# Optimization experiments

Measured on AMD Instinct MI355X. Metric: run time of the kernel, lower is better.

The kernel has to match this reference:

```python
import jax, jax.numpy as jnp
import numpy as np

D_MODEL = 768; D_STATE = 64; D_CONV = 7; EXPAND = 2; HEADDIM = 64; NGROUPS = 1; CHUNK = 256
D_INNER = EXPAND * D_MODEL                                      # 1536
NHEADS = D_INNER // HEADDIM                                     # 24
D_IN_PROJ = 2 * D_INNER + 2 * NGROUPS * D_STATE + 2 * NHEADS    # 3248
CONV_DIM = D_INNER + 2 * NGROUPS * D_STATE                      # 1664
BATCH, SEQLEN = 2, 4096
EPS = 1e-5


def setup_inputs() -> dict:
    key = jax.random.key(0)
    ks = jax.random.split(key, 8)
    w = lambda k, shape, s=0.02: jax.random.normal(k, shape, jnp.float32) * s
    # dt in [1e-3, 1e-1], dt_bias = softplus^{-1}(dt)
    dt0 = jnp.exp(jax.random.uniform(ks[3], (NHEADS,)) * (np.log(0.1) - np.log(0.001)) + np.log(0.001))
    return {
        "x": jax.random.normal(ks[0], (BATCH, SEQLEN, D_MODEL), jnp.float32),
        "ln_w": jnp.ones((D_MODEL,), jnp.float32),
        "ln_b": jnp.zeros((D_MODEL,), jnp.float32),
        "in_proj_w": w(ks[1], (D_IN_PROJ, D_MODEL)),
        "conv_w": w(ks[2], (CONV_DIM, D_CONV), 0.2),
        "conv_b": jnp.zeros((CONV_DIM,), jnp.float32),
        "dt_bias": dt0 + jnp.log(-jnp.expm1(-dt0)),
        "A_log": jnp.log(jax.random.uniform(ks[4], (NHEADS,), minval=1.0, maxval=16.0)),
        "D": jnp.ones((NHEADS,), jnp.float32),
        "fc_D_w": w(ks[5], (NHEADS, D_INNER)),
        "rms_w": jnp.ones((D_INNER,), jnp.float32),
        "out_proj_w": w(ks[6], (D_MODEL, D_INNER)),
    }


def _segsum(a):
    # a: (..., T) -> (..., T, T) lower-triangular segment sums, -inf above diagonal
    T = a.shape[-1]
    cs = jnp.cumsum(a, -1)
    ss = cs[..., :, None] - cs[..., None, :]
    return jnp.where(jnp.tril(jnp.ones((T, T), bool)), ss, -jnp.inf)


def _ssd(X, A, Bm, Cm):
    # Chunked SSD scan (mamba_chunk_scan_combined, D=None, z=None, ngroups=1).
    # X: (b,l,h,p) already scaled by dt; A: (b,l,h) = dt*A_head; Bm,Cm: (b,l,n)
    b, l, h, p = X.shape
    c = l // CHUNK
    X = X.reshape(b, c, CHUNK, h, p)
    A = A.reshape(b, c, CHUNK, h).transpose(0, 3, 1, 2)  # (b,h,c,l)
    Bm = Bm.reshape(b, c, CHUNK, D_STATE)
    Cm = Cm.reshape(b, c, CHUNK, D_STATE)
    A_cum = jnp.cumsum(A, -1)
    Lmat = jnp.exp(_segsum(A))                                      # (b,h,c,l,s)
    Y_diag = jnp.einsum("bcln,bcsn,bhcls,bcshp->bclhp", Cm, Bm, Lmat, X)
    decay_states = jnp.exp(A_cum[..., -1:] - A_cum)                 # (b,h,c,l)
    states = jnp.einsum("bcln,bhcl,bclhp->bchpn", Bm, decay_states, X)
    A_chunk = jnp.pad(A_cum[..., -1], ((0, 0), (0, 0), (1, 0)))     # (b,h,c+1)
    decay_chunk = jnp.exp(_segsum(A_chunk))                         # (b,h,c+1,c+1)
    all_states = jnp.concatenate([jnp.zeros_like(states[:, :1]), states], 1)
    prev = jnp.einsum("bhzc,bchpn->bzhpn", decay_chunk, all_states)[:, :-1]
    Y_off = jnp.einsum("bcln,bchpn,bhcl->bclhp", Cm, prev, jnp.exp(A_cum))
    return (Y_diag + Y_off).reshape(b, l, h, p)


def _dwconv_causal(x, w, b):
    # x: (B,L,C), w: (C,K); torch Conv1d(padding=K-1) then [:, :L] == causal conv
    xp = jnp.pad(x, ((0, 0), (D_CONV - 1, 0), (0, 0))).transpose(0, 2, 1)
    y = jax.lax.conv_general_dilated(xp, w[:, None, :], (1,), "VALID",
                                     feature_group_count=CONV_DIM,
                                     dimension_numbers=("NCH", "OIH", "NCH"))
    return y.transpose(0, 2, 1) + b


def _forward(x, ln_w, ln_b, in_proj_w, conv_w, conv_b, dt_bias, A_log, D, fc_D_w, rms_w, out_proj_w):
    B, L, _ = x.shape
    # pre-LayerNorm
    mu = jnp.mean(x, -1, keepdims=True)
    var = jnp.mean((x - mu) ** 2, -1, keepdims=True)
    u = (x - mu) * jax.lax.rsqrt(var + EPS) * ln_w + ln_b
    # input projection -> z | xBC | dt_fw,dt_bw
    zxbcdt = u @ in_proj_w.T
    z = zxbcdt[..., :D_INNER]
    xBC = zxbcdt[..., D_INNER:D_INNER + CONV_DIM]
    dt2 = zxbcdt[..., -2 * NHEADS:]
    dt = jnp.concatenate([dt2[..., :NHEADS], jnp.flip(dt2[..., NHEADS:], 1)], 0)  # (2B,L,H)
    dt = jax.nn.softplus(dt + dt_bias)
    A = -jnp.exp(A_log)
    # causal depthwise conv + SiLU
    xBC = jax.nn.silu(_dwconv_causal(xBC, conv_w, conv_b))
    xs = xBC[..., :D_INNER]
    Bm = xBC[..., D_INNER:D_INNER + D_STATE]
    Cm = xBC[..., D_INNER + D_STATE:]
    x_og = xs
    cat2 = lambda t: jnp.concatenate([t, jnp.flip(t, 1)], 0)  # fwd + reversed copy
    X = cat2(xs).reshape(2 * B, L, NHEADS, HEADDIM) * dt[..., None]
    y = _ssd(X, dt * A, cat2(Bm), cat2(Cm)).reshape(2 * B, L, D_INNER)
    # quasiseparable combine: shift each direction by one, zero the boundary
    y = jnp.roll(y, 1, axis=1).at[:, 0, :].set(0.0)
    y = y[:B] + jnp.flip(y[B:], 1)
    # data-dependent diagonal term
    Dterm = x_og @ fc_D_w.T + D                                 # (B,L,H)
    y = y + x_og * jnp.repeat(Dterm, HEADDIM, axis=-1)
    # gated RMSNorm
    y = y * jax.nn.silu(z)
    y = y * jax.lax.rsqrt(jnp.mean(y * y, -1, keepdims=True) + EPS) * rms_w
    # out projection + residual (dropout=0 -> identity)
    return y @ out_proj_w.T + x


def reference(x, ln_w, ln_b, in_proj_w, conv_w, conv_b, dt_bias, A_log, D, fc_D_w, rms_w, out_proj_w):
    return _forward(x, ln_w, ln_b, in_proj_w, conv_w, conv_b, dt_bias, A_log, D, fc_D_w, rms_w, out_proj_w)
```

## Files before the change

kernel.cpp:

```cpp
#include <hip/hip_runtime.h>
#include <hip/hip_bf16.h>
#include <cstdint>
#include <cstddef>

typedef __hip_bfloat16 bf16;
typedef __attribute__((ext_vector_type(8))) short short8;
typedef __attribute__((ext_vector_type(4))) float f32x4;

#define B_   2
#define L_   4096
#define DM_  768
#define DI_  1536
#define NH_  24
#define HD_  64
#define DS_  64
#define CH_  256
#define NC_  16
#define CD_  1664
#define DIP_ 3248
#define NPAD_ 3328
#define EPS_ 1e-5f

#define ROWS_ (B_*L_)
#define BB4_  (2*B_)

#define LDT  72

__device__ __forceinline__ float b2f(bf16 v) { return __bfloat162float(v); }
__device__ __forceinline__ bf16  f2b(float v) { return __float2bfloat16(v); }
__device__ __forceinline__ float sb2f(short s) {
    bf16 t; __builtin_memcpy(&t, &s, 2); return __bfloat162float(t);
}
__device__ __forceinline__ short f2s(float v) {
    bf16 t = __float2bfloat16(v); short s; __builtin_memcpy(&s, &t, 2); return s;
}
__device__ __forceinline__ void gl_lds16(const void* g, void* l) {
    __builtin_amdgcn_global_load_lds((const __attribute__((address_space(1))) unsigned int*)g,
                                     (__attribute__((address_space(3))) unsigned int*)l,
                                     16, 0, 0);
}

__global__ __launch_bounds__(256) void cast_f2b(const float* __restrict__ s,
                                                bf16* __restrict__ d, int n) {
    int i = (blockIdx.x * 256 + threadIdx.x) * 4;
    if (i + 3 < n) {
        float4 v = *(const float4*)(s + i);
        d[i]   = f2b(v.x); d[i+1] = f2b(v.y);
        d[i+2] = f2b(v.z); d[i+3] = f2b(v.w);
    } else {
        for (int k = i; k < n; k++) d[k] = f2b(s[k]);
    }
}

__global__ __launch_bounds__(256) void cast_pad_inproj(const float* __restrict__ s,
                                                       bf16* __restrict__ d) {
    int i = (blockIdx.x * 256 + threadIdx.x) * 4;
    const int nsrc = DIP_ * DM_;
    const int ntot = NPAD_ * DM_;
    if (i >= ntot) return;
    if (i + 3 < nsrc) {
        float4 v = *(const float4*)(s + i);
        d[i]   = f2b(v.x); d[i+1] = f2b(v.y);
        d[i+2] = f2b(v.z); d[i+3] = f2b(v.w);
    } else {
        for (int k = i; k < i + 4 && k < ntot; k++)
            d[k] = (k < nsrc) ? f2b(s[k]) : f2b(0.f);
    }
}

__global__ __launch_bounds__(256) void ln_kernel(const float* __restrict__ x,
                                                 const float* __restrict__ w,
                                                 const float* __restrict__ bb,
                                                 bf16* __restrict__ u) {
    int row = blockIdx.x, tid = threadIdx.x;
    const float* xr = x + (size_t)row * DM_;
    float v0 = xr[tid], v1 = xr[tid + 256], v2 = xr[tid + 512];
    float s = v0 + v1 + v2;
    float q = v0*v0 + v1*v1 + v2*v2;
    for (int off = 32; off > 0; off >>= 1) {
        s += __shfl_down(s, off);
        q += __shfl_down(q, off);
    }
    __shared__ float rs[4], rq[4];
    __shared__ float mean_s, rstd_s;
    int lane = tid & 63, wid = tid >> 6;
    if (!lane) { rs[wid] = s; rq[wid] = q; }
    __syncthreads();
    if (!tid) {
        float S = rs[0]+rs[1]+rs[2]+rs[3];
        float Q = rq[0]+rq[1]+rq[2]+rq[3];
        float mu = S / (float)DM_;
        float var = Q / (float)DM_ - mu*mu;
        mean_s = mu; rstd_s = rsqrtf(var + EPS_);
    }
    __syncthreads();
    float mu = mean_s, rstd = rstd_s;
    bf16* ur = u + (size_t)row * DM_;
    ur[tid]       = f2b((v0 - mu) * rstd * w[tid]       + bb[tid]);
    ur[tid + 256] = f2b((v1 - mu) * rstd * w[tid + 256] + bb[tid + 256]);
    ur[tid + 512] = f2b((v2 - mu) * rstd * w[tid + 512] + bb[tid + 512]);
}

__global__ __launch_bounds__(256) void gemm_gl_inproj(const bf16* __restrict__ A,
                                                      const bf16* __restrict__ W,
                                                      bf16* __restrict__ zbuf,
                                                      bf16* __restrict__ xbc,
                                                      float* __restrict__ dtr) {
    __shared__ short As[128 * 32];
    __shared__ short Ws[128 * 32];
    int tid = threadIdx.x;
    int wave = tid >> 6, lane = tid & 63;
    int wm = (wave >> 1) * 64, wn = (wave & 1) * 64;
    int bm = blockIdx.y * 128, bn = blockIdx.x * 128;
    int fr = lane & 15, g = lane >> 4;
    const int K = DM_;
    int srow = lane >> 2;
    int scol = ((lane & 3) ^ ((lane >> 3) & 3)) * 8;
    int rsl = (g ^ ((fr >> 1) & 3)) * 8;
    const short* Ag = (const short*)A;
    const short* Wg = (const short*)W;
    f32x4 acc[4][4] = {};
    for (int k0 = 0; k0 < K; k0 += 32) {
        __syncthreads();
        #pragma unroll
        for (int q = 0; q < 2; q++) {
            gl_lds16(Ag + (size_t)(bm + q*64 + wave*16 + srow) * K + k0 + scol,
                     &As[(q*64 + wave*16) * 32]);
            gl_lds16(Wg + (size_t)(bn + q*64 + wave*16 + srow) * K + k0 + scol,
                     &Ws[(q*64 + wave*16) * 32]);
        }
        __syncthreads();
        short8 af[4], wf[4];
        #pragma unroll
        for (int i = 0; i < 4; i++)
            af[i] = *(const short8*)&As[(wm + i*16 + fr)*32 + rsl];
        #pragma unroll
        for (int j = 0; j < 4; j++)
            wf[j] = *(const short8*)&Ws[(wn + j*16 + fr)*32 + rsl];
        #pragma unroll
        for (int i = 0; i < 4; i++)
            #pragma unroll
            for (int j = 0; j < 4; j++)
                acc[i][j] = __builtin_amdgcn_mfma_f32_16x16x32_bf16(af[i], wf[j], acc[i][j], 0, 0, 0);
    }
    int rg = (lane >> 4) * 4;
    #pragma unroll
    for (int i = 0; i < 4; i++) {
        int mrow = bm + wm + i*16 + rg;
        #pragma unroll
        for (int j = 0; j < 4; j++) {
            int ncol = bn + wn + j*16 + fr;
            #pragma unroll
            for (int r = 0; r < 4; r++) {
                float v = acc[i][j][r];
                int m = mrow + r;
                if (ncol < DI_)            zbuf[(size_t)m * DI_ + ncol] = f2b(v);
                else if (ncol < DI_ + CD_) xbc[(size_t)m * CD_ + (ncol - DI_)] = f2b(v);
                else if (ncol < DIP_)      dtr[(size_t)m * 48 + (ncol - DI_ - CD_)] = v;
            }
        }
    }
}

__global__ __launch_bounds__(256) void gemm_gl_out(const bf16* __restrict__ A,
                                                   const bf16* __restrict__ W,
                                                   const float* __restrict__ resid,
                                                   float* __restrict__ C) {
    __shared__ short As[128 * 32];
    __shared__ short Ws[128 * 32];
    int tid = threadIdx.x;
    int wave = tid >> 6, lane = tid & 63;
    int wm = (wave >> 1) * 64, wn = (wave & 1) * 64;
    int bm = blockIdx.y * 128, bn = blockIdx.x * 128;
    int fr = lane & 15, g = lane >> 4;
    const int K = DI_;
    int srow = lane >> 2;
    int scol = ((lane & 3) ^ ((lane >> 3) & 3)) * 8;
    int rsl = (g ^ ((fr >> 1) & 3)) * 8;
    const short* Ag = (const short*)A;
    const short* Wg = (const short*)W;
    f32x4 acc[4][4] = {};
    for (int k0 = 0; k0 < K; k0 += 32) {
        __syncthreads();
        #pragma unroll
        for (int q = 0; q < 2; q++) {
            gl_lds16(Ag + (size_t)(bm + q*64 + wave*16 + srow) * K + k0 + scol,
                     &As[(q*64 + wave*16) * 32]);
            gl_lds16(Wg + (size_t)(bn + q*64 + wave*16 + srow) * K + k0 + scol,
                     &Ws[(q*64 + wave*16) * 32]);
        }
        __syncthreads();
        short8 af[4], wf[4];
        #pragma unroll
        for (int i = 0; i < 4; i++)
            af[i] = *(const short8*)&As[(wm + i*16 + fr)*32 + rsl];
        #pragma unroll
        for (int j = 0; j < 4; j++)
            wf[j] = *(const short8*)&Ws[(wn + j*16 + fr)*32 + rsl];
        #pragma unroll
        for (int i = 0; i < 4; i++)
            #pragma unroll
            for (int j = 0; j < 4; j++)
                acc[i][j] = __builtin_amdgcn_mfma_f32_16x16x32_bf16(af[i], wf[j], acc[i][j], 0, 0, 0);
    }
    int rg = (lane >> 4) * 4;
    #pragma unroll
    for (int i = 0; i < 4; i++) {
        int mrow = bm + wm + i*16 + rg;
        #pragma unroll
        for (int j = 0; j < 4; j++) {
            int ncol = bn + wn + j*16 + fr;
            #pragma unroll
            for (int r = 0; r < 4; r++) {
                int m = mrow + r;
                C[(size_t)m * DM_ + ncol] = acc[i][j][r] + resid[(size_t)m * DM_ + ncol];
            }
        }
    }
}

__global__ __launch_bounds__(256) void conv_kernel(const bf16* __restrict__ xbc,
                                                   const float* __restrict__ cw,
                                                   const float* __restrict__ cb,
                                                   bf16* __restrict__ out) {
    int g = blockIdx.x * 256 + threadIdx.x;
    int cg = g % 208;
    int tq = g / 208;
    int b = tq >> 10;
    int t0 = (tq & 1023) * 4;
    int c8 = cg * 8;
    const short* src = (const short*)xbc + (size_t)(b * L_) * CD_ + c8;

    float w[7][8], acc[4][8];
    #pragma unroll
    for (int k = 0; k < 8; k++) {
        #pragma unroll
        for (int j = 0; j < 7; j++) w[j][k] = cw[(c8 + k) * 7 + j];
        float bias = cb[c8 + k];
        #pragma unroll
        for (int q = 0; q < 4; q++) acc[q][k] = bias;
    }
    #pragma unroll
    for (int m = 0; m < 10; m++) {
        int tt = t0 - 6 + m;
        float row[8];
        if (tt >= 0) {
            short8 v = *(const short8*)(src + (size_t)tt * CD_);
            #pragma unroll
            for (int k = 0; k < 8; k++) row[k] = sb2f(v[k]);
        } else {
            #pragma unroll
            for (int k = 0; k < 8; k++) row[k] = 0.f;
        }
        #pragma unroll
        for (int q = 0; q < 4; q++) {
            int j = m - q;
            if (j >= 0 && j < 7) {
                #pragma unroll
                for (int k = 0; k < 8; k++) acc[q][k] += row[k] * w[j][k];
            }
        }
    }
    #pragma unroll
    for (int q = 0; q < 4; q++) {
        short8 o;
        #pragma unroll
        for (int k = 0; k < 8; k++) {
            float a = acc[q][k];
            a = a / (1.f + __expf(-a));
            o[k] = f2s(a);
        }
        *(short8*)((short*)out + (size_t)(b * L_ + t0 + q) * CD_ + c8) = o;
    }
}

__global__ __launch_bounds__(256) void dt_kernel(const float* __restrict__ dtr,
                                                 const float* __restrict__ dt_bias,
                                                 float* __restrict__ dt4) {
    int idx = blockIdx.x * 256 + threadIdx.x;
    if (idx >= BB4_ * L_ * NH_) return;
    int h = idx % NH_;
    int t = (idx / NH_) % L_;
    int bbx = idx / (NH_ * L_);
    int bp = bbx & 1;
    float raw;
    if (bbx < 2) raw = dtr[((size_t)(bp * L_ + t)) * 48 + h];
    else         raw = dtr[((size_t)(bp * L_ + (L_ - 1 - t))) * 48 + NH_ + h];
    float v = raw + dt_bias[h];
    float dt = (v > 20.f) ? v : log1pf(__expf(v));
    dt4[idx] = dt;
}

__global__ __launch_bounds__(256) void scan_kernel(const float* __restrict__ dt4,
                                                   const float* __restrict__ A_log,
                                                   float* __restrict__ Acum) {
    int bid = blockIdx.x;
    int c  = bid % NC_;
    int h  = (bid / NC_) % NH_;
    int bbx = bid / (NC_ * NH_);
    int l = threadIdx.x;
    float Ah = -__expf(A_log[h]);
    float val = dt4[((size_t)(bbx * L_) + c * CH_ + l) * NH_ + h] * Ah;
    __shared__ float sc[256];
    sc[l] = val; __syncthreads();
    for (int off = 1; off < 256; off <<= 1) {
        float t = (l >= off) ? sc[l - off] : 0.f;
        __syncthreads();
        sc[l] += t;
        __syncthreads();
    }
    Acum[(size_t)bid * CH_ + l] = sc[l];
}

__global__ __launch_bounds__(256) void xt_kernel(const bf16* __restrict__ conv,
                                                 const float* __restrict__ dt4,
                                                 bf16* __restrict__ XT,
                                                 bf16* __restrict__ BT) {
    int bid = blockIdx.x;
    int hh = bid % 25;
    int c  = (bid / 25) % NC_;
    int bbx = bid / (25 * NC_);
    int bp = bbx & 1;
    bool flip = bbx >= 2;
    bool isB = (hh == NH_);
    int coff = isB ? DI_ : hh * HD_;
    int tid = threadIdx.x;
    __shared__ short tile[64][72];
    short* dstb = (short*)(isB ? BT : XT);
    size_t rowbase = isB ? (size_t)(bbx * 64) : (size_t)((bbx * NH_ + hh) * 64);
    for (int lt = 0; lt < 4; lt++) {
        __syncthreads();
        #pragma unroll
        for (int it = 0; it < 2; it++) {
            int li = tid + it * 256;
            int r = li >> 3, seg = (li & 7) * 8;
            int t = c * CH_ + lt * 64 + r;
            int tt = flip ? (L_ - 1 - t) : t;
            short8 v = *(const short8*)((const short*)conv + (size_t)(bp * L_ + tt) * CD_ + coff + seg);
            if (!isB) {
                float dtv = dt4[((size_t)(bbx * L_) + t) * NH_ + hh];
                #pragma unroll
                for (int k = 0; k < 8; k++) v[k] = f2s(sb2f(v[k]) * dtv);
            }
            *(short8*)&tile[r][seg] = v;
        }
        __syncthreads();
        #pragma unroll
        for (int it = 0; it < 2; it++) {
            int li = tid + it * 256;
            int p = li >> 3, seg = (li & 7) * 8;
            short8 o;
            #pragma unroll
            for (int k = 0; k < 8; k++) o[k] = tile[seg + k][p];
            *(short8*)(dstb + (rowbase + p) * L_ + c * CH_ + lt * 64 + seg) = o;
        }
    }
}

__global__ __launch_bounds__(256) void states_kernel(const bf16* __restrict__ XT,
                                                     const bf16* __restrict__ BT,
                                                     const float* __restrict__ Acum,
                                                     bf16* __restrict__ states) {
    int bid = blockIdx.x;
    int h = bid % NH_;
    int c = (bid / NH_) % NC_;
    int bbx = bid / (NH_ * NC_);
    int tid = threadIdx.x;
    int wave = tid >> 6, lane = tid & 63;
    int wr = wave >> 1, wc = wave & 1;
    int fr = lane & 15, kg = (lane >> 4) * 8, rg = (lane >> 4) * 4;
    size_t abase = ((size_t)(bbx * NH_ + h) * NC_ + c) * CH_;
    __shared__ float dec[256];
    {
        float Atot = Acum[abase + CH_ - 1];
        dec[tid] = __expf(Atot - Acum[abase + tid]);
    }
    __syncthreads();
    const short* xbase = (const short*)XT + (size_t)((bbx * NH_ + h) * 64) * L_ + c * CH_;
    const short* bbase = (const short*)BT + (size_t)(bbx * 64) * L_ + c * CH_;
    f32x4 acc[2][2] = {};
    for (int lt = 0; lt < 4; lt++) {
        #pragma unroll
        for (int ks = 0; ks < 2; ks++) {
            int l0 = lt * 64 + ks * 32 + kg;
            float d[8];
            #pragma unroll
            for (int k = 0; k < 8; k++) d[k] = dec[l0 + k];
            short8 af[2], wf[2];
            #pragma unroll
            for (int i = 0; i < 2; i++)
                af[i] = *(const short8*)(xbase + (size_t)(wr*32 + i*16 + fr) * L_ + l0);
            #pragma unroll
            for (int j = 0; j < 2; j++) {
                short8 raw = *(const short8*)(bbase + (size_t)(wc*32 + j*16 + fr) * L_ + l0);
                #pragma unroll
                for (int k = 0; k < 8; k++) raw[k] = f2s(sb2f(raw[k]) * d[k]);
                wf[j] = raw;
            }
            #pragma unroll
            for (int i = 0; i < 2; i++)
                #pragma unroll
                for (int j = 0; j < 2; j++)
                    acc[i][j] = __builtin_amdgcn_mfma_f32_16x16x32_bf16(af[i], wf[j], acc[i][j], 0, 0, 0);
        }
    }
    size_t sbase = (size_t)bid * 4096;
    #pragma unroll
    for (int i = 0; i < 2; i++)
        #pragma unroll
        for (int j = 0; j < 2; j++)
            #pragma unroll
            for (int r = 0; r < 4; r++) {
                int p = wr*32 + i*16 + rg + r;
                int n = wc*32 + j*16 + fr;
                states[sbase + p*64 + n] = f2b(acc[i][j][r]);
            }
}

__global__ __launch_bounds__(256) void chunkscan_kernel(bf16* __restrict__ sp,
                                                        const float* __restrict__ Acum) {
    int bid = blockIdx.x;
    int h = bid % NH_;
    int bbx = bid / NH_;
    int tid = threadIdx.x;
    float run[16];
    #pragma unroll
    for (int k = 0; k < 16; k++) run[k] = 0.f;
    for (int c = 0; c < NC_; c++) {
        float Tc = Acum[((size_t)(bbx * NH_ + h) * NC_ + c) * CH_ + CH_ - 1];
        float ec = __expf(Tc);
        size_t base = ((size_t)(bbx * NC_ + c) * NH_ + h) * 4096;
        #pragma unroll
        for (int k = 0; k < 16; k++) {
            size_t e = tid + k * 256;
            float sv = b2f(sp[base + e]);
            sp[base + e] = f2b(run[k]);
            run[k] = run[k] * ec + sv;
        }
    }
}

__global__ __launch_bounds__(256) void ydiag_kernel(const bf16* __restrict__ conv,
                                                    const bf16* __restrict__ XT,
                                                    const float* __restrict__ Acum,
                                                    const bf16* __restrict__ prev,
                                                    bf16* __restrict__ yf,
                                                    bf16* __restrict__ yb) {
    int bid = blockIdx.x;
    int lt = bid & 3;
    int q  = bid >> 2;
    int h  = q % NH_;
    int r2 = q / NH_;
    int c  = r2 % NC_;
    int bbx = r2 / NC_;
    int bp = bbx & 1;
    bool flip = bbx >= 2;
    int tid = threadIdx.x;
    int wave = tid >> 6, lane = tid & 63;
    int wr = wave >> 1, wc = wave & 1;
    int fr = lane & 15, kg = (lane >> 4) * 8, rg = (lane >> 4) * 4;
    size_t abase = ((size_t)(bbx * NH_ + h) * NC_ + c) * CH_;

    __shared__ short Gt[64 * LDT];
    __shared__ float aL[64], aS[64];
    if (tid < 64) aL[tid] = Acum[abase + lt * 64 + tid];

    short8 cf[2][2];
    #pragma unroll
    for (int i = 0; i < 2; i++) {
        int l = wr*32 + i*16 + fr;
        int t = c * CH_ + lt * 64 + l;
        int tt = flip ? (L_ - 1 - t) : t;
        const short* crow = (const short*)conv + (size_t)(bp * L_ + tt) * CD_ + DI_ + DS_;
        #pragma unroll
        for (int ks = 0; ks < 2; ks++)
            cf[i][ks] = *(const short8*)(crow + ks*32 + kg);
    }

    f32x4 acc[2][2] = {};
    size_t pbase = ((size_t)(bbx * NC_ + c) * NH_ + h) * 4096;
    #pragma unroll
    for (int ks = 0; ks < 2; ks++) {
        #pragma unroll
        for (int j = 0; j < 2; j++) {
            short8 pf = *(const short8*)((const short*)prev + pbase + (size_t)(wc*32 + j*16 + fr)*64 + ks*32 + kg);
            #pragma unroll
            for (int i = 0; i < 2; i++)
                acc[i][j] = __builtin_amdgcn_mfma_f32_16x16x32_bf16(cf[i][ks], pf, acc[i][j], 0, 0, 0);
        }
    }
    __syncthreads();
    #pragma unroll
    for (int i = 0; i < 2; i++)
        #pragma unroll
        for (int r = 0; r < 4; r++) {
            float e = __expf(aL[wr*32 + i*16 + rg + r]);
            #pragma unroll
            for (int j = 0; j < 2; j++) acc[i][j][r] *= e;
        }

    const short* xbase = (const short*)XT + (size_t)((bbx * NH_ + h) * 64) * L_ + c * CH_;

    for (int st = 0; st <= lt; st++) {
        if (tid < 64) aS[tid] = Acum[abase + st * 64 + tid];
        f32x4 gacc[2][2] = {};
        #pragma unroll
        for (int j = 0; j < 2; j++) {
            int s = wc*32 + j*16 + fr;
            int t = c * CH_ + st * 64 + s;
            int tt = flip ? (L_ - 1 - t) : t;
            const short* brow = (const short*)conv + (size_t)(bp * L_ + tt) * CD_ + DI_;
            #pragma unroll
            for (int ks = 0; ks < 2; ks++) {
                short8 bfv = *(const short8*)(brow + ks*32 + kg);
                #pragma unroll
                for (int i = 0; i < 2; i++)
                    gacc[i][j] = __builtin_amdgcn_mfma_f32_16x16x32_bf16(cf[i][ks], bfv, gacc[i][j], 0, 0, 0);
            }
        }
        __syncthreads();
        #pragma unroll
        for (int i = 0; i < 2; i++)
            #pragma unroll
            for (int j = 0; j < 2; j++)
                #pragma unroll
                for (int r = 0; r < 4; r++) {
                    int ll = wr*32 + i*16 + rg + r;
                    int ss = wc*32 + j*16 + fr;
                    bool valid = (st < lt) || (ll >= ss);
                    float gv = valid ? gacc[i][j][r] * __expf(aL[ll] - aS[ss]) : 0.f;
                    Gt[ll * LDT + ss] = f2s(gv);
                }
        __syncthreads();
        #pragma unroll
        for (int ks = 0; ks < 2; ks++) {
            short8 gf[2], xf[2];
            #pragma unroll
            for (int i = 0; i < 2; i++)
                gf[i] = *(const short8*)&Gt[(wr*32 + i*16 + fr)*LDT + ks*32 + kg];
            #pragma unroll
            for (int j = 0; j < 2; j++)
                xf[j] = *(const short8*)(xbase + (size_t)(wc*32 + j*16 + fr)*L_ + st*64 + ks*32 + kg);
            #pragma unroll
            for (int i = 0; i < 2; i++)
                #pragma unroll
                for (int j = 0; j < 2; j++)
                    acc[i][j] = __builtin_amdgcn_mfma_f32_16x16x32_bf16(gf[i], xf[j], acc[i][j], 0, 0, 0);
        }
        __syncthreads();
    }

    bf16* dst = flip ? yb : yf;
    #pragma unroll
    for (int i = 0; i < 2; i++)
        #pragma unroll
        for (int r = 0; r < 4; r++) {
            int l = wr*32 + i*16 + rg + r;
            int t = c * CH_ + lt * 64 + l;
            #pragma unroll
            for (int j = 0; j < 2; j++) {
                int p = wc*32 + j*16 + fr;
                dst[((size_t)(bp * L_) + t) * DI_ + h * HD_ + p] = f2b(acc[i][j][r]);
            }
        }
}

__global__ __launch_bounds__(256) void combine_kernel(const bf16* __restrict__ yf,
                                                      const bf16* __restrict__ yb,
                                                      const bf16* __restrict__ conv,
                                                      const bf16* __restrict__ zbuf,
                                                      const float* __restrict__ fcD,
                                                      const float* __restrict__ Dvec,
                                                      const float* __restrict__ rms_w,
                                                      bf16* __restrict__ ybuf) {
    int row = blockIdx.x;
    int b = row >> 12;
    int t = row & (L_ - 1);
    int tid = threadIdx.x;
    __shared__ float xog_s[DI_];
    __shared__ float dterm_s[NH_];
    __shared__ float rs[4];
    __shared__ float scale_s;
    float yv[6], xog[6], zv[6];
    const bf16* convrow = conv + (size_t)row * CD_;
    const bf16* zrow = zbuf + (size_t)row * DI_;
    const bf16* yfr = (t > 0) ? (yf + (size_t)(row - 1) * DI_) : nullptr;
    const bf16* ybr = (t < L_ - 1) ? (yb + ((size_t)(b * L_) + (L_ - 2 - t)) * DI_) : nullptr;
    #pragma unroll
    for (int k = 0; k < 6; k++) {
        int d = tid + k * 256;
        float xo = b2f(convrow[d]);
        xog[k] = xo; xog_s[d] = xo;
        zv[k] = b2f(zrow[d]);
        float y1 = yfr ? b2f(yfr[d]) : 0.f;
        float y2 = ybr ? b2f(ybr[d]) : 0.f;
        yv[k] = y1 + y2;
    }
    __syncthreads();
    int wid = tid >> 6, lane = tid & 63;
    for (int hh = 0; hh < 6; hh++) {
        int h = wid * 6 + hh;
        float s = 0.f;
        #pragma unroll
        for (int k = 0; k < 24; k++) {
            int d = lane + k * 64;
            s += xog_s[d] * fcD[(size_t)h * DI_ + d];
        }
        for (int off = 32; off > 0; off >>= 1) s += __shfl_down(s, off);
        if (!lane) dterm_s[h] = s + Dvec[h];
    }
    __syncthreads();
    float ss = 0.f;
    #pragma unroll
    for (int k = 0; k < 6; k++) {
        int d = tid + k * 256;
        int h = d >> 6;
        float y = yv[k] + xog[k] * dterm_s[h];
        float z = zv[k];
        y *= z / (1.f + __expf(-z));
        yv[k] = y;
        ss += y * y;
    }
    for (int off = 32; off > 0; off >>= 1) ss += __shfl_down(ss, off);
    if (!lane) rs[wid] = ss;
    __syncthreads();
    if (!tid) scale_s = rsqrtf((rs[0]+rs[1]+rs[2]+rs[3]) / (float)DI_ + EPS_);
    __syncthreads();
    float sc = scale_s;
    bf16* yrow = ybuf + (size_t)row * DI_;
    #pragma unroll
    for (int k = 0; k < 6; k++) {
        int d = tid + k * 256;
        yrow[d] = f2b(yv[k] * sc * rms_w[d]);
    }
}

extern "C" void kernel_launch(void* const* d_in, const int* in_sizes, int n_in,
                              void* d_out, int out_size, void* d_ws, size_t ws_size,
                              hipStream_t stream) {
    const float* x        = (const float*)d_in[0];
    const float* ln_w     = (const float*)d_in[1];
    const float* ln_b     = (const float*)d_in[2];
    const float* in_proj  = (const float*)d_in[3];
    const float* conv_w   = (const float*)d_in[4];
    const float* conv_b   = (const float*)d_in[5];
    const float* dt_bias  = (const float*)d_in[6];
    const float* A_log    = (const float*)d_in[7];
    const float* Dvec     = (const float*)d_in[8];
    const float* fc_D_w   = (const float*)d_in[9];
    const float* rms_w    = (const float*)d_in[10];
    const float* out_proj = (const float*)d_in[11];
    float* out = (float*)d_out;

    uint8_t* base = (uint8_t*)d_ws;
    size_t off = 0;
    auto alloc = [&](size_t bytes) -> void* {
        void* p = base + off;
        off += (bytes + 255) & ~(size_t)255;
        return p;
    };
    bf16*  buf_z    = (bf16*) alloc((size_t)ROWS_ * DI_ * 2);
    uint8_t* regA   = (uint8_t*)alloc((size_t)ROWS_ * CD_ * 2);
    float* buf_dtr  = (float*)alloc((size_t)ROWS_ * 48 * 4);
    bf16*  buf_conv = (bf16*) alloc((size_t)ROWS_ * CD_ * 2);
    float* buf_dt   = (float*)alloc((size_t)BB4_ * L_ * NH_ * 4);
    float* buf_acum = (float*)alloc((size_t)BB4_ * NH_ * NC_ * CH_ * 4);
    uint8_t* regB   = (uint8_t*)alloc((size_t)ROWS_ * DM_ * 4);
    bf16*  buf_yb   = (bf16*) alloc((size_t)B_ * L_ * DI_ * 2);
    bf16*  w_in_bf  = (bf16*) alloc((size_t)NPAD_ * DM_ * 2);
    bf16*  w_out_bf = (bf16*) alloc((size_t)DM_ * DI_ * 2);
    bf16*  buf_XT   = (bf16*) alloc((size_t)BB4_ * NH_ * 64 * L_ * 2);
    bf16*  buf_BT   = (bf16*) alloc((size_t)BB4_ * 64 * L_ * 2);

    bf16*  buf_xbc  = (bf16*)regA;
    bf16*  buf_sp   = (bf16*)regA;
    bf16*  buf_y    = (bf16*)regA;
    bf16*  buf_u    = (bf16*)regB;
    bf16*  buf_yf   = (bf16*)regB;

    cast_pad_inproj<<<(NPAD_ * DM_ / 4 + 255) / 256, 256, 0, stream>>>(in_proj, w_in_bf);
    cast_f2b<<<(DM_ * DI_ / 4 + 255) / 256, 256, 0, stream>>>(out_proj, w_out_bf, DM_ * DI_);
    ln_kernel<<<ROWS_, 256, 0, stream>>>(x, ln_w, ln_b, buf_u);
    gemm_gl_inproj<<<dim3(NPAD_ / 128, ROWS_ / 128), 256, 0, stream>>>(
        buf_u, w_in_bf, buf_z, buf_xbc, buf_dtr);
    conv_kernel<<<(ROWS_ / 4) * (CD_ / 8) / 256, 256, 0, stream>>>(buf_xbc, conv_w, conv_b, buf_conv);
    dt_kernel<<<(BB4_ * L_ * NH_) / 256, 256, 0, stream>>>(buf_dtr, dt_bias, buf_dt);
    scan_kernel<<<BB4_ * NH_ * NC_, 256, 0, stream>>>(buf_dt, A_log, buf_acum);
    xt_kernel<<<BB4_ * NC_ * 25, 256, 0, stream>>>(buf_conv, buf_dt, buf_XT, buf_BT);
    states_kernel<<<BB4_ * NC_ * NH_, 256, 0, stream>>>(buf_XT, buf_BT, buf_acum, buf_sp);
    chunkscan_kernel<<<BB4_ * NH_, 256, 0, stream>>>(buf_sp, buf_acum);
    ydiag_kernel<<<BB4_ * NC_ * NH_ * 4, 256, 0, stream>>>(buf_conv, buf_XT, buf_acum, buf_sp, buf_yf, buf_yb);
    combine_kernel<<<ROWS_, 256, 0, stream>>>(buf_yf, buf_yb, buf_conv, buf_z, fc_D_w, Dvec, rms_w, buf_y);
    gemm_gl_out<<<dim3(DM_ / 128, ROWS_ / 128), 256, 0, stream>>>(
        buf_y, w_out_bf, x, out);
}
```

Measured before the change: 545.0 us.

## Swizzle block order, widen conv time tile, prefetch operands in ydiag loop

Conv now gives each thread 8 timesteps instead of 4, reusing loaded rows over a wider window and halving the grid. The conv, xt, states and ydiag kernels remap block indices with a stride-8 swizzle, likely to spread neighbouring blocks across the XCDs. In ydiag, the per-row and per-column cumulative-A values move from shared memory into registers, which removes one barrier. The next B fragment and the X fragments are prefetched before the MFMA work so the global loads overlap with compute, at the cost of more registers.

```diff
diff --git a/kernel.cpp b/kernel.cpp
--- a/kernel.cpp
+++ b/kernel.cpp
@@ -223,25 +223,27 @@
                                                    const float* __restrict__ cw,
                                                    const float* __restrict__ cb,
                                                    bf16* __restrict__ out) {
-    int g = blockIdx.x * 256 + threadIdx.x;
+    int bid0 = blockIdx.x;
+    int bid = (bid0 & 7) * 104 + (bid0 >> 3);
+    int g = bid * 256 + threadIdx.x;
     int cg = g % 208;
     int tq = g / 208;
-    int b = tq >> 10;
-    int t0 = (tq & 1023) * 4;
+    int b = tq >> 9;
+    int t0 = (tq & 511) * 8;
     int c8 = cg * 8;
     const short* src = (const short*)xbc + (size_t)(b * L_) * CD_ + c8;
 
-    float w[7][8], acc[4][8];
+    float w[7][8], acc[8][8];
     #pragma unroll
     for (int k = 0; k < 8; k++) {
         #pragma unroll
         for (int j = 0; j < 7; j++) w[j][k] = cw[(c8 + k) * 7 + j];
         float bias = cb[c8 + k];
         #pragma unroll
-        for (int q = 0; q < 4; q++) acc[q][k] = bias;
-    }
-    #pragma unroll
-    for (int m = 0; m < 10; m++) {
+        for (int q = 0; q < 8; q++) acc[q][k] = bias;
+    }
+    #pragma unroll
+    for (int m = 0; m < 14; m++) {
         int tt = t0 - 6 + m;
         float row[8];
         if (tt >= 0) {
@@ -253,7 +255,7 @@
             for (int k = 0; k < 8; k++) row[k] = 0.f;
         }
         #pragma unroll
-        for (int q = 0; q < 4; q++) {
+        for (int q = 0; q < 8; q++) {
             int j = m - q;
             if (j >= 0 && j < 7) {
                 #pragma unroll
@@ -262,7 +264,7 @@
         }
     }
     #pragma unroll
-    for (int q = 0; q < 4; q++) {
+    for (int q = 0; q < 8; q++) {
         short8 o;
         #pragma unroll
         for (int k = 0; k < 8; k++) {
@@ -316,7 +318,8 @@
                                                  const float* __restrict__ dt4,
                                                  bf16* __restrict__ XT,
                                                  bf16* __restrict__ BT) {
-    int bid = blockIdx.x;
+    int bid0 = blockIdx.x;
+    int bid = (bid0 & 7) * 200 + (bid0 >> 3);
     int hh = bid % 25;
     int c  = (bid / 25) % NC_;
     int bbx = bid / (25 * NC_);
@@ -361,7 +364,8 @@
                                                      const bf16* __restrict__ BT,
                                                      const float* __restrict__ Acum,
                                                      bf16* __restrict__ states) {
-    int bid = blockIdx.x;
+    int bid0 = blockIdx.x;
+    int bid = (bid0 & 7) * 192 + (bid0 >> 3);
     int h = bid % NH_;
     int c = (bid / NH_) % NC_;
     int bbx = bid / (NH_ * NC_);
@@ -446,7 +450,8 @@
                                                     const bf16* __restrict__ prev,
                                                     bf16* __restrict__ yf,
                                                     bf16* __restrict__ yb) {
-    int bid = blockIdx.x;
+    int bid0 = blockIdx.x;
+    int bid = (bid0 & 7) * 768 + (bid0 >> 3);
     int lt = bid & 3;
     int q  = bid >> 2;
     int h  = q % NH_;
@@ -462,8 +467,13 @@
     size_t abase = ((size_t)(bbx * NH_ + h) * NC_ + c) * CH_;
 
     __shared__ short Gt[64 * LDT];
-    __shared__ float aL[64], aS[64];
-    if (tid < 64) aL[tid] = Acum[abase + lt * 64 + tid];
+
+    float aLv[2][4];
+    #pragma unroll
+    for (int i = 0; i < 2; i++)
+        #pragma unroll
+        for (int r = 0; r < 4; r++)
+            aLv[i][r] = Acum[abase + lt * 64 + wr*32 + i*16 + rg + r];
 
     short8 cf[2][2];
     #pragma unroll
@@ -489,36 +499,61 @@
                 acc[i][j] = __builtin_amdgcn_mfma_f32_16x16x32_bf16(cf[i][ks], pf, acc[i][j], 0, 0, 0);
         }
     }
-    __syncthreads();
     #pragma unroll
     for (int i = 0; i < 2; i++)
         #pragma unroll
         for (int r = 0; r < 4; r++) {
-            float e = __expf(aL[wr*32 + i*16 + rg + r]);
+            float e = __expf(aLv[i][r]);
             #pragma unroll
             for (int j = 0; j < 2; j++) acc[i][j][r] *= e;
         }
 
     const short* xbase = (const short*)XT + (size_t)((bbx * NH_ + h) * 64) * L_ + c * CH_;
 
+    short8 bf_c[2][2];
+    float aSc[2];
+    #pragma unroll
+    for (int j = 0; j < 2; j++) {
+        int s = wc*32 + j*16 + fr;
+        int t = c * CH_ + s;
+        int tt = flip ? (L_ - 1 - t) : t;
+        const short* brow = (const short*)conv + (size_t)(bp * L_ + tt) * CD_ + DI_;
+        #pragma unroll
+        for (int ks = 0; ks < 2; ks++)
+            bf_c[j][ks] = *(const short8*)(brow + ks*32 + kg);
+        aSc[j] = Acum[abase + s];
+    }
+
     for (int st = 0; st <= lt; st++) {
-        if (tid < 64) aS[tid] = Acum[abase + st * 64 + tid];
+        short8 xf[2][2];
+        #pragma unroll
+        for (int j = 0; j < 2; j++)
+            #pragma unroll
+            for (int ks = 0; ks < 2; ks++)
+                xf[j][ks] = *(const short8*)(xbase + (size_t)(wc*32 + j*16 + fr)*L_ + st*64 + ks*32 + kg);
+        short8 bf_n[2][2];
+        float aSn[2];
+        if (st < lt) {
+            #pragma unroll
+            for (int j = 0; j < 2; j++) {
+                int s = wc*32 + j*16 + fr;
+                int t = c * CH_ + (st+1) * 64 + s;
+                int tt = flip ? (L_ - 1 - t) : t;
+                const short* brow = (const short*)conv + (size_t)(bp * L_ + tt) * CD_ + DI_;
+                #pragma unroll
+                for (int ks = 0; ks < 2; ks++)
+                    bf_n[j][ks] = *(const short8*)(brow + ks*32 + kg);
+                aSn[j] = Acum[abase + (st+1)*64 + s];
+            }
+        }
         f32x4 gacc[2][2] = {};
         #pragma unroll
-        for (int j = 0; j < 2; j++) {
-            int s = wc*32 + j*16 + fr;
-            int t = c * CH_ + st * 64 + s;
-            int tt = flip ? (L_ - 1 - t) : t;
-            const short* brow = (const short*)conv + (size_t)(bp * L_ + tt) * CD_ + DI_;
-            #pragma unroll
-            for (int ks = 0; ks < 2; ks++) {
-                short8 bfv = *(const short8*)(brow + ks*32 + kg);
+        for (int ks = 0; ks < 2; ks++)
+            #pragma unroll
+            for (int j = 0; j < 2; j++)
                 #pragma unroll
                 for (int i = 0; i < 2; i++)
-                    gacc[i][j] = __builtin_amdgcn_mfma_f32_16x16x32_bf16(cf[i][ks], bfv, gacc[i][j], 0, 0, 0);
-            }
-        }
-        __syncthreads();
+                    gacc[i][j] = __builtin_amdgcn_mfma_f32_16x16x32_bf16(cf[i][ks], bf_c[j][ks], gacc[i][j], 0, 0, 0);
         #pragma unroll
         for (int i = 0; i < 2; i++)
             #pragma unroll
@@ -528,26 +563,31 @@
                     int ll = wr*32 + i*16 + rg + r;
                     int ss = wc*32 + j*16 + fr;
                     bool valid = (st < lt) || (ll >= ss);
-                    float gv = valid ? gacc[i][j][r] * __expf(aL[ll] - aS[ss]) : 0.f;
+                    float gv = valid ? gacc[i][j][r] * __expf(aLv[i][r] - aSc[j]) : 0.f;
                     Gt[ll * LDT + ss] = f2s(gv);
                 }
         __syncthreads();
         #pragma unroll
         for (int ks = 0; ks < 2; ks++) {
-            short8 gf[2], xf[2];
+            short8 gf[2];
             #pragma unroll
             for (int i = 0; i < 2; i++)
                 gf[i] = *(const short8*)&Gt[(wr*32 + i*16 + fr)*LDT + ks*32 + kg];
             #pragma unroll
-            for (int j = 0; j < 2; j++)
-                xf[j] = *(const short8*)(xbase + (size_t)(wc*32 + j*16 + fr)*L_ + st*64 + ks*32 + kg);
-            #pragma unroll
             for (int i = 0; i < 2; i++)
                 #pragma unroll
                 for (int j = 0; j < 2; j++)
-                    acc[i][j] = __builtin_amdgcn_mfma_f32_16x16x32_bf16(gf[i], xf[j], acc[i][j], 0, 0, 0);
-        }
-        __syncthreads();
+                    acc[i][j] = __builtin_amdgcn_mfma_f32_16x16x32_bf16(gf[i], xf[j][ks], acc[i][j], 0, 0, 0);
+        }
+        __syncthreads();
+        if (st < lt) {
+            #pragma unroll
+            for (int j = 0; j < 2; j++) {
+                #pragma unroll
+                for (int ks = 0; ks < 2; ks++) bf_c[j][ks] = bf_n[j][ks];
+                aSc[j] = aSn[j];
+            }
+        }
     }
 
     bf16* dst = flip ? yb : yf;
@@ -683,7 +723,7 @@
     ln_kernel<<<ROWS_, 256, 0, stream>>>(x, ln_w, ln_b, buf_u);
     gemm_gl_inproj<<<dim3(NPAD_ / 128, ROWS_ / 128), 256, 0, stream>>>(
         buf_u, w_in_bf, buf_z, buf_xbc, buf_dtr);
-    conv_kernel<<<(ROWS_ / 4) * (CD_ / 8) / 256, 256, 0, stream>>>(buf_xbc, conv_w, conv_b, buf_conv);
+    conv_kernel<<<832, 256, 0, stream>>>(buf_xbc, conv_w, conv_b, buf_conv);
     dt_kernel<<<(BB4_ * L_ * NH_) / 256, 256, 0, stream>>>(buf_dtr, dt_bias, buf_dt);
     scan_kernel<<<BB4_ * NH_ * NC_, 256, 0, stream>>>(buf_dt, A_log, buf_acum);
     xt_kernel<<<BB4_ * NC_ * 25, 256, 0, stream>>>(buf_conv, buf_dt, buf_XT, buf_BT);
```

Measured after the change: 524.5 us. 1.04x faster.
